# Kernel optimization log

Hardware: AMD Instinct MI355X
Metric: run time of the kernel (lower is better)

Reference implementation:

```python
import jax, jax.numpy as jnp
import numpy as np
from jax import lax

B, T, K = 16, 8, 64
COUT, CIN, KH, KW = 128, 128, 5, 5
H, W = 64, 64
PAD = 2  # p=2 in batch_conv -> same spatial size for 5x5


def setup_inputs() -> dict:
    key = jax.random.key(0)
    k1, k2, k3 = jax.random.split(key, 3)
    x = jax.random.normal(k1, (B, CIN, H, W), dtype=jnp.float32)
    task_features = jax.random.normal(k2, (B, T, K), dtype=jnp.float32)
    # learned weight bank (kaiming-uniform in torch; scaled normal is fine for a reference)
    fan_in = CIN * KH * KW
    weights = jax.random.normal(k3, (K, COUT, CIN, KH, KW), dtype=jnp.float32) / np.sqrt(fan_in)
    return {"x": x, "task_features": task_features, "weights": weights}


def reference(x, task_features, weights):
    # infer_params: per-demonstration weighted sum over the K weight bank,
    # then mean over demonstrations T. Fused into one contraction:
    #   sum_t sum_k tf[b,t,k] * W[k,o,c,i,j] / T
    layer_params = jnp.einsum('btk,kocij->bocij', task_features, weights) / T  # (B,Cout,Cin,kh,kw)

    # batch_conv: per-example conv2d with padding 2 (group=B pattern)
    def conv_one(xi, wi):
        # xi: (Cin,H,W), wi: (Cout,Cin,kh,kw)
        return lax.conv_general_dilated(
            xi[None], wi, window_strides=(1, 1),
            padding=[(PAD, PAD), (PAD, PAD)],
            dimension_numbers=('NCHW', 'OIHW', 'NCHW'))[0]

    y = jax.vmap(conv_one)(x, layer_params)  # (B, Cout, H, W)
    return y
```

## Files before the change

### kernel.cpp

```cpp
#include <hip/hip_runtime.h>

#define B_    16
#define T_    8
#define K_    64
#define COUT  128
#define CIN   128
#define H_    64
#define W_    64
#define WSZ   (COUT*CIN*5*5)

typedef __bf16 bf16x8 __attribute__((ext_vector_type(8)));
typedef float  f32x4  __attribute__((ext_vector_type(4)));

static __device__ __forceinline__ unsigned short f2bf(float f) {
    unsigned int u = __builtin_bit_cast(unsigned int, f);
    unsigned int r = (u + 0x7FFFu + ((u >> 16) & 1u)) >> 16;
    return (unsigned short)r;
}

__global__ __launch_bounds__(256) void prep_kernel(const float* __restrict__ Wb,
                                                   const float* __restrict__ tf,
                                                   const float* __restrict__ x,
                                                   unsigned short* __restrict__ lpF,
                                                   unsigned short* __restrict__ xT) {
    __shared__ __align__(16) char smem[30720];
    int tid = threadIdx.x;

    if (blockIdx.x < 512) {
        float* cs          = (float*)smem;
        unsigned short* lt = (unsigned short*)(smem + 4096);

        int o = blockIdx.x >> 2;
        int s = blockIdx.x & 3;

        {
            int idx = tid;
#pragma unroll
            for (int r = 0; r < 4; ++r, idx += 256) {
                int b = idx >> 6, k = idx & 63;
                float sum = 0.f;
#pragma unroll
                for (int t = 0; t < T_; ++t) sum += tf[(b * T_ + t) * K_ + k];
                cs[idx] = sum * 0.125f;
            }
        }
        __syncthreads();

        if (tid < 200) {
            int base = o * 3200 + s * 800 + tid * 4;
            float4 acc[B_];
#pragma unroll
            for (int b = 0; b < B_; ++b) acc[b] = make_float4(0.f, 0.f, 0.f, 0.f);

#pragma unroll 4
            for (int k = 0; k < K_; ++k) {
                const float4 wv = *(const float4*)(Wb + (size_t)k * WSZ + base);
#pragma unroll
                for (int b = 0; b < B_; ++b) {
                    float c = cs[b * K_ + k];
                    acc[b].x += c * wv.x;
                    acc[b].y += c * wv.y;
                    acc[b].z += c * wv.z;
                    acc[b].w += c * wv.w;
                }
            }
            unsigned int* ltw = (unsigned int*)lt;
#pragma unroll
            for (int b = 0; b < B_; ++b) {
                unsigned int p0 = f2bf(acc[b].x) | ((unsigned int)f2bf(acc[b].y) << 16);
                unsigned int p1 = f2bf(acc[b].z) | ((unsigned int)f2bf(acc[b].w) << 16);
                ltw[b * 400 + tid * 2]     = p0;
                ltw[b * 400 + tid * 2 + 1] = p1;
            }
        }
        __syncthreads();

        int wm = o >> 6, mt = (o >> 4) & 3, n16 = o & 15;
        for (int it = tid; it < 1600; it += 256) {
            int b = it / 100;
            int r = it - b * 100;
            int tap = r >> 2;
            int quad = r & 3;
            unsigned short v[8];
#pragma unroll
            for (int j = 0; j < 8; ++j)
                v[j] = lt[b * 800 + (quad * 8 + j) * 25 + tap];
            size_t off = (size_t)b * 409600
                       + (size_t)((((tap * 4 + s) * 2 + wm) * 4 + mt) * 512
                                  + quad * 128 + n16 * 8);
            *(uint4*)(lpF + off) = *(const uint4*)v;
        }
    } else {
        unsigned short* ls = (unsigned short*)smem;
        int q = blockIdx.x - 512;
        int b = q >> 6, h = q & 63;

        int w = tid & 63, cb = tid >> 6;
        const float* xp = x + (((size_t)(b * CIN + cb * 32) * H_ + h) * W_) + w;
#pragma unroll
        for (int p = 0; p < 16; ++p) {
            float f0 = xp[(size_t)(2 * p) * (H_ * W_)];
            float f1 = xp[(size_t)(2 * p + 1) * (H_ * W_)];
            unsigned int v = f2bf(f0) | ((unsigned int)f2bf(f1) << 16);
            *(unsigned int*)&ls[w * 136 + cb * 32 + 2 * p] = v;
        }
        __syncthreads();

        unsigned short* xTb = xT + ((size_t)(b * 64 + h) * 64) * 128;
        int chunk = tid & 15, wr = tid >> 4;
#pragma unroll
        for (int pass = 0; pass < 4; ++pass) {
            int ww = pass * 16 + wr;
            uint4 v = *(const uint4*)&ls[ww * 136 + chunk * 8];
            *(uint4*)&xTb[ww * 128 + chunk * 8] = v;
        }
    }
}

__global__ __launch_bounds__(256) void conv_mfma(const unsigned short* __restrict__ xT,
                                                 const unsigned short* __restrict__ lpF,
                                                 float* __restrict__ out) {
    int bid = blockIdx.x;
    int b  = (bid & 7) | (((bid >> 3) & 1) << 3);
    int h0 = (bid >> 4) << 1;

    int tid  = threadIdx.x;
    int lane = tid & 63, wid = tid >> 6;
    int wm = wid & 1, wn = wid >> 1;
    int n16 = lane & 15, quad = lane >> 4;

    __shared__ __align__(16) unsigned short xs[408 * 40];

    f32x4 acc[4][4];
#pragma unroll
    for (int mt = 0; mt < 4; ++mt)
#pragma unroll
        for (int nt = 0; nt < 4; ++nt) acc[mt][nt] = (f32x4){0.f, 0.f, 0.f, 0.f};

    const unsigned short* xTb = xT + (size_t)b * (64 * 64 * 128);
    const unsigned short* lpW = lpF + (size_t)b * 409600 + wm * 2048 + lane * 8;

#define LOAD_FRAGS(A, Bf, tap) do {                                          \
    int i_ = (tap) / 5, j_ = (tap) - 5 * (i_);                               \
    const unsigned short* ap_ = lpW + (tap) * 16384 + kcB;                   \
    A[0] = *(const bf16x8*)(ap_);                                            \
    A[1] = *(const bf16x8*)(ap_ + 512);                                      \
    A[2] = *(const bf16x8*)(ap_ + 1024);                                     \
    A[3] = *(const bf16x8*)(ap_ + 1536);                                     \
    const unsigned short* bp_ = &xs[(((wn + i_) * 68) + n16 + j_) * 40 + quad * 8]; \
    Bf[0] = *(const bf16x8*)(bp_);                                           \
    Bf[1] = *(const bf16x8*)(bp_ + 16 * 40);                                 \
    Bf[2] = *(const bf16x8*)(bp_ + 32 * 40);                                 \
    Bf[3] = *(const bf16x8*)(bp_ + 48 * 40);                                 \
} while (0)

#define DO_MFMA(av, bv) do {                                                 \
    _Pragma("unroll") for (int mt = 0; mt < 4; ++mt)                         \
    _Pragma("unroll") for (int nt = 0; nt < 4; ++nt)                         \
        acc[mt][nt] = __builtin_amdgcn_mfma_f32_16x16x32_bf16(               \
            (av)[mt], (bv)[nt], acc[mt][nt], 0, 0, 0);                       \
} while (0)

    for (int kc = 0; kc < 4; ++kc) {
        int kcOff = kc * 32;
        int kcB   = kc * 4096;
        __syncthreads();
        for (int sIdx = tid; sIdx < 408; sIdx += 256) {
            unsigned int su = (unsigned int)sIdx;
            int rr = su / 68u;
            int ww = su - rr * 68u;
            int gr = h0 - 2 + rr, gw = ww - 2;
            uint4* dst = (uint4*)&xs[sIdx * 40];
            if ((unsigned)gr < 64u && (unsigned)gw < 64u) {
                const uint4* src = (const uint4*)(xTb + (((size_t)gr * 64 + gw) * 128 + kcOff));
                dst[0] = src[0]; dst[1] = src[1]; dst[2] = src[2]; dst[3] = src[3];
            } else {
                uint4 z = {0u, 0u, 0u, 0u};
                dst[0] = z; dst[1] = z; dst[2] = z; dst[3] = z;
            }
        }
        __syncthreads();

        bf16x8 a0[4], b0[4], a1[4], b1[4];
        LOAD_FRAGS(a0, b0, 0);
        for (int t = 0; t < 24; t += 2) {
            LOAD_FRAGS(a1, b1, t + 1);
            DO_MFMA(a0, b0);
            LOAD_FRAGS(a0, b0, t + 2);
            DO_MFMA(a1, b1);
        }
        DO_MFMA(a0, b0);
    }

    float* outb = out + (size_t)b * (COUT * H_ * W_) + (size_t)(h0 + wn) * W_;
#pragma unroll
    for (int mt = 0; mt < 4; ++mt) {
#pragma unroll
        for (int nt = 0; nt < 4; ++nt) {
#pragma unroll
            for (int r = 0; r < 4; ++r) {
                int o = wm * 64 + mt * 16 + quad * 4 + r;
                int w = nt * 16 + n16;
                outb[(size_t)o * (H_ * W_) + w] = acc[mt][nt][r];
            }
        }
    }
#undef LOAD_FRAGS
#undef DO_MFMA
}

extern "C" void kernel_launch(void* const* d_in, const int* in_sizes, int n_in,
                              void* d_out, int out_size, void* d_ws, size_t ws_size,
                              hipStream_t stream) {
    const float* x  = (const float*)d_in[0];
    const float* tf = (const float*)d_in[1];
    const float* Wb = (const float*)d_in[2];
    float* out = (float*)d_out;

    unsigned short* lpF = (unsigned short*)d_ws;
    unsigned short* xT  = lpF + (size_t)B_ * 409600;

    prep_kernel<<<1536, 256, 0, stream>>>(Wb, tf, x, lpF, xT);
    conv_mfma  <<<512,  256, 0, stream>>>(xT, lpF, out);
}
```

Baseline: 241.1 us.

## Fuse prep and conv kernels into one persistent launch with grid barrier

Merges the weight-mixing/transpose prep kernel and the MFMA conv kernel into a single 512-block launch. Each block first does one slice of weight mixing and two rows of the input transpose, then waits at a software grid barrier (an atomic counter with sleep) before running its conv tile. This removes the second launch and the gap between kernels. In exchange it requires all 512 blocks to be co-resident (launch bounds of 4 blocks per CU) and adds the spin barrier, which deadlocks if residency fails. The counter also relies on every block decrementing it at exit to reset it for the next call.

```diff
diff --git a/kernel.cpp b/kernel.cpp
--- a/kernel.cpp
+++ b/kernel.cpp
@@ -8,9 +8,12 @@
 #define H_    64
 #define W_    64
 #define WSZ   (COUT*CIN*5*5)
+#define NBLK  512
 
 typedef __bf16 bf16x8 __attribute__((ext_vector_type(8)));
 typedef float  f32x4  __attribute__((ext_vector_type(4)));
+
+__device__ int g_cnt = 0;
 
 static __device__ __forceinline__ unsigned short f2bf(float f) {
     unsigned int u = __builtin_bit_cast(unsigned int, f);
@@ -18,33 +21,40 @@
     return (unsigned short)r;
 }
 
-__global__ __launch_bounds__(256) void prep_kernel(const float* __restrict__ Wb,
-                                                   const float* __restrict__ tf,
-                                                   const float* __restrict__ x,
-                                                   unsigned short* __restrict__ lpF,
-                                                   unsigned short* __restrict__ xT) {
-    __shared__ __align__(16) char smem[30720];
+static __device__ __forceinline__ unsigned int pack2(float lo, float hi) {
+    return (unsigned int)f2bf(lo) | ((unsigned int)f2bf(hi) << 16);
+}
+
+__global__ __launch_bounds__(256, 4) void fused_kernel(const float* __restrict__ Wb,
+                                                       const float* __restrict__ tf,
+                                                       const float* __restrict__ x,
+                                                       unsigned short* __restrict__ lpF,
+                                                       unsigned short* __restrict__ xT,
+                                                       float* __restrict__ out) {
+    __shared__ __align__(16) char smem[32640];
     int tid = threadIdx.x;
-
-    if (blockIdx.x < 512) {
+    int bid = blockIdx.x;
+
+    {
+        float* cs = (float*)smem;
+        int idx = tid;
+#pragma unroll
+        for (int r = 0; r < 4; ++r, idx += 256) {
+            int b = idx >> 6, k = idx & 63;
+            float sum = 0.f;
+#pragma unroll
+            for (int t = 0; t < T_; ++t) sum += tf[(b * T_ + t) * K_ + k];
+            cs[idx] = sum * 0.125f;
+        }
+    }
+    __syncthreads();
+
+    {
         float* cs          = (float*)smem;
         unsigned short* lt = (unsigned short*)(smem + 4096);
 
-        int o = blockIdx.x >> 2;
-        int s = blockIdx.x & 3;
-
-        {
-            int idx = tid;
-#pragma unroll
-            for (int r = 0; r < 4; ++r, idx += 256) {
-                int b = idx >> 6, k = idx & 63;
-                float sum = 0.f;
-#pragma unroll
-                for (int t = 0; t < T_; ++t) sum += tf[(b * T_ + t) * K_ + k];
-                cs[idx] = sum * 0.125f;
-            }
-        }
-        __syncthreads();
+        int o = bid >> 2;
+        int s = bid & 3;
 
         if (tid < 200) {
             int base = o * 3200 + s * 800 + tid * 4;
@@ -67,10 +77,8 @@
             unsigned int* ltw = (unsigned int*)lt;
 #pragma unroll
             for (int b = 0; b < B_; ++b) {
-                unsigned int p0 = f2bf(acc[b].x) | ((unsigned int)f2bf(acc[b].y) << 16);
-                unsigned int p1 = f2bf(acc[b].z) | ((unsigned int)f2bf(acc[b].w) << 16);
-                ltw[b * 400 + tid * 2]     = p0;
-                ltw[b * 400 + tid * 2 + 1] = p1;
+                ltw[b * 400 + tid * 2]     = pack2(acc[b].x, acc[b].y);
+                ltw[b * 400 + tid * 2 + 1] = pack2(acc[b].z, acc[b].w);
             }
         }
         __syncthreads();
@@ -90,55 +98,65 @@
                                   + quad * 128 + n16 * 8);
             *(uint4*)(lpF + off) = *(const uint4*)v;
         }
-    } else {
+    }
+    __syncthreads();
+
+    {
         unsigned short* ls = (unsigned short*)smem;
-        int q = blockIdx.x - 512;
-        int b = q >> 6, h = q & 63;
-
-        int w = tid & 63, cb = tid >> 6;
-        const float* xp = x + (((size_t)(b * CIN + cb * 32) * H_ + h) * W_) + w;
-#pragma unroll
-        for (int p = 0; p < 16; ++p) {
-            float f0 = xp[(size_t)(2 * p) * (H_ * W_)];
-            float f1 = xp[(size_t)(2 * p + 1) * (H_ * W_)];
-            unsigned int v = f2bf(f0) | ((unsigned int)f2bf(f1) << 16);
-            *(unsigned int*)&ls[w * 136 + cb * 32 + 2 * p] = v;
-        }
-        __syncthreads();
-
-        unsigned short* xTb = xT + ((size_t)(b * 64 + h) * 64) * 128;
-        int chunk = tid & 15, wr = tid >> 4;
-#pragma unroll
-        for (int pass = 0; pass < 4; ++pass) {
-            int ww = pass * 16 + wr;
-            uint4 v = *(const uint4*)&ls[ww * 136 + chunk * 8];
-            *(uint4*)&xTb[ww * 128 + chunk * 8] = v;
-        }
-    }
-}
-
-__global__ __launch_bounds__(256) void conv_mfma(const unsigned short* __restrict__ xT,
-                                                 const unsigned short* __restrict__ lpF,
-                                                 float* __restrict__ out) {
-    int bid = blockIdx.x;
-    int b  = (bid & 7) | (((bid >> 3) & 1) << 3);
-    int h0 = (bid >> 4) << 1;
-
-    int tid  = threadIdx.x;
-    int lane = tid & 63, wid = tid >> 6;
-    int wm = wid & 1, wn = wid >> 1;
-    int n16 = lane & 15, quad = lane >> 4;
-
-    __shared__ __align__(16) unsigned short xs[408 * 40];
-
-    f32x4 acc[4][4];
-#pragma unroll
-    for (int mt = 0; mt < 4; ++mt)
-#pragma unroll
-        for (int nt = 0; nt < 4; ++nt) acc[mt][nt] = (f32x4){0.f, 0.f, 0.f, 0.f};
-
-    const unsigned short* xTb = xT + (size_t)b * (64 * 64 * 128);
-    const unsigned short* lpW = lpF + (size_t)b * 409600 + wm * 2048 + lane * 8;
+#pragma unroll
+        for (int u = 0; u < 2; ++u) {
+            int q = bid * 2 + u;
+            int b = q >> 6, h = q & 63;
+
+            int w = tid & 63, cb = tid >> 6;
+            const float* xp = x + (((size_t)(b * CIN + cb * 32) * H_ + h) * W_) + w;
+#pragma unroll
+            for (int p = 0; p < 16; ++p) {
+                float f0 = xp[(size_t)(2 * p) * (H_ * W_)];
+                float f1 = xp[(size_t)(2 * p + 1) * (H_ * W_)];
+                *(unsigned int*)&ls[w * 136 + cb * 32 + 2 * p] = pack2(f0, f1);
+            }
+            __syncthreads();
+
+            unsigned short* xTb = xT + ((size_t)(b * 64 + h) * 64) * 128;
+            int chunk = tid & 15, wr = tid >> 4;
+#pragma unroll
+            for (int pass = 0; pass < 4; ++pass) {
+                int ww = pass * 16 + wr;
+                uint4 v = *(const uint4*)&ls[ww * 136 + chunk * 8];
+                *(uint4*)&xTb[ww * 128 + chunk * 8] = v;
+            }
+            __syncthreads();
+        }
+    }
+
+    __threadfence();
+    __syncthreads();
+    if (tid == 0) {
+        atomicAdd(&g_cnt, 1);
+        while (atomicAdd(&g_cnt, 0) < NBLK) __builtin_amdgcn_s_sleep(2);
+    }
+    __syncthreads();
+    __threadfence();
+
+    {
+        int b  = (bid & 7) | (((bid >> 3) & 1) << 3);
+        int h0 = (bid >> 4) << 1;
+
+        int lane = tid & 63, wid = tid >> 6;
+        int wm = wid & 1, wn = wid >> 1;
+        int n16 = lane & 15, quad = lane >> 4;
+
+        unsigned short* xs = (unsigned short*)smem;
+
+        f32x4 acc[4][4];
+#pragma unroll
+        for (int mt = 0; mt < 4; ++mt)
+#pragma unroll
+            for (int nt = 0; nt < 4; ++nt) acc[mt][nt] = (f32x4){0.f, 0.f, 0.f, 0.f};
+
+        const unsigned short* xTb = xT + (size_t)b * (64 * 64 * 128);
+        const unsigned short* lpW = lpF + (size_t)b * 409600 + wm * 2048 + lane * 8;
 
 #define LOAD_FRAGS(A, Bf, tap) do {                                          \
     int i_ = (tap) / 5, j_ = (tap) - 5 * (i_);                               \
@@ -161,52 +179,55 @@
             (av)[mt], (bv)[nt], acc[mt][nt], 0, 0, 0);                       \
 } while (0)
 
-    for (int kc = 0; kc < 4; ++kc) {
-        int kcOff = kc * 32;
-        int kcB   = kc * 4096;
-        __syncthreads();
-        for (int sIdx = tid; sIdx < 408; sIdx += 256) {
-            unsigned int su = (unsigned int)sIdx;
-            int rr = su / 68u;
-            int ww = su - rr * 68u;
-            int gr = h0 - 2 + rr, gw = ww - 2;
-            uint4* dst = (uint4*)&xs[sIdx * 40];
-            if ((unsigned)gr < 64u && (unsigned)gw < 64u) {
-                const uint4* src = (const uint4*)(xTb + (((size_t)gr * 64 + gw) * 128 + kcOff));
-                dst[0] = src[0]; dst[1] = src[1]; dst[2] = src[2]; dst[3] = src[3];
-            } else {
-                uint4 z = {0u, 0u, 0u, 0u};
-                dst[0] = z; dst[1] = z; dst[2] = z; dst[3] = z;
-            }
-        }
-        __syncthreads();
-
-        bf16x8 a0[4], b0[4], a1[4], b1[4];
-        LOAD_FRAGS(a0, b0, 0);
-        for (int t = 0; t < 24; t += 2) {
-            LOAD_FRAGS(a1, b1, t + 1);
+        for (int kc = 0; kc < 4; ++kc) {
+            int kcOff = kc * 32;
+            int kcB   = kc * 4096;
+            __syncthreads();
+            for (int sIdx = tid; sIdx < 408; sIdx += 256) {
+                unsigned int su = (unsigned int)sIdx;
+                int rr = su / 68u;
+                int ww = su - rr * 68u;
+                int gr = h0 - 2 + rr, gw = ww - 2;
+                uint4* dst = (uint4*)&xs[sIdx * 40];
+                if ((unsigned)gr < 64u && (unsigned)gw < 64u) {
+                    const uint4* src = (const uint4*)(xTb + (((size_t)gr * 64 + gw) * 128 + kcOff));
+                    dst[0] = src[0]; dst[1] = src[1]; dst[2] = src[2]; dst[3] = src[3];
+                } else {
+                    uint4 z = {0u, 0u, 0u, 0u};
+                    dst[0] = z; dst[1] = z; dst[2] = z; dst[3] = z;
+                }
+            }
+            __syncthreads();
+
+            bf16x8 a0[4], b0[4], a1[4], b1[4];
+            LOAD_FRAGS(a0, b0, 0);
+            for (int t = 0; t < 24; t += 2) {
+                LOAD_FRAGS(a1, b1, t + 1);
+                DO_MFMA(a0, b0);
+                LOAD_FRAGS(a0, b0, t + 2);
+                DO_MFMA(a1, b1);
+            }
             DO_MFMA(a0, b0);
-            LOAD_FRAGS(a0, b0, t + 2);
-            DO_MFMA(a1, b1);
-        }
-        DO_MFMA(a0, b0);
-    }
-
-    float* outb = out + (size_t)b * (COUT * H_ * W_) + (size_t)(h0 + wn) * W_;
-#pragma unroll
-    for (int mt = 0; mt < 4; ++mt) {
-#pragma unroll
-        for (int nt = 0; nt < 4; ++nt) {
-#pragma unroll
-            for (int r = 0; r < 4; ++r) {
-                int o = wm * 64 + mt * 16 + quad * 4 + r;
-                int w = nt * 16 + n16;
-                outb[(size_t)o * (H_ * W_) + w] = acc[mt][nt][r];
-            }
-        }
-    }
+        }
+
+        float* outb = out + (size_t)b * (COUT * H_ * W_) + (size_t)(h0 + wn) * W_;
+#pragma unroll
+        for (int mt = 0; mt < 4; ++mt) {
+#pragma unroll
+            for (int nt = 0; nt < 4; ++nt) {
+#pragma unroll
+                for (int r = 0; r < 4; ++r) {
+                    int o = wm * 64 + mt * 16 + quad * 4 + r;
+                    int w = nt * 16 + n16;
+                    outb[(size_t)o * (H_ * W_) + w] = acc[mt][nt][r];
+                }
+            }
+        }
 #undef LOAD_FRAGS
 #undef DO_MFMA
+    }
+
+    if (tid == 0) atomicSub(&g_cnt, 1);
 }
 
 extern "C" void kernel_launch(void* const* d_in, const int* in_sizes, int n_in,
@@ -220,6 +241,5 @@
     unsigned short* lpF = (unsigned short*)d_ws;
     unsigned short* xT  = lpF + (size_t)B_ * 409600;
 
-    prep_kernel<<<1536, 256, 0, stream>>>(Wb, tf, x, lpF, xT);
-    conv_mfma  <<<512,  256, 0, stream>>>(xT, lpF, out);
-}
+    fused_kernel<<<NBLK, 256, 0, stream>>>(Wb, tf, x, lpF, xT, out);
+}
```

Result: slower. 533.2 us (+121.1%).
